# Kernel optimization log

Hardware: AMD Instinct MI355X
Metric: run time of the kernel (lower is better)

## Reference

```python
import jax, jax.numpy as jnp
import numpy as np

NH, D, MULT, NLAYER = 8, 512, 32, 3
N_INT = D * MULT // NH  # 2048 sparse-code dim per head
EPS = 1e-5
THETA = 2.0 ** 16
NUM_CLASSES = 2


def _ln(x):
    # LayerNorm over last dim, no affine (elementwise_affine=False), biased var
    m = jnp.mean(x, axis=-1, keepdims=True)
    v = jnp.mean((x - m) ** 2, axis=-1, keepdims=True)
    return (x - m) * jax.lax.rsqrt(v + EPS)


def _rotate_half(x):
    x1, x2 = jnp.split(x, 2, axis=-1)
    return jnp.concatenate((-x2, x1), axis=-1)


def _attn(Qs, V):
    # Qs: [B,nh,T,N] ReLU-sparse codes (Q == K), V: [B,1,T,D] raw hidden
    T = Qs.shape[2]
    half = 1.0 / (THETA ** (jnp.arange(0, N_INT, 2, dtype=jnp.float32) / N_INT))
    freqs = jnp.concatenate((half, half))                      # [N]
    ph = jnp.arange(T, dtype=jnp.float32)[:, None] * freqs[None, :]  # [T,N]
    QR = Qs * jnp.cos(ph) + _rotate_half(Qs) * jnp.sin(ph)
    scores = jnp.einsum('bhtn,bhsn->bhts', QR, QR)             # no softmax, no scaling
    mask = jnp.tril(jnp.ones((T, T), dtype=scores.dtype), k=-1)  # strictly causal
    scores = scores * mask
    return jnp.einsum('bhts,bsd->bhtd', scores, V[:, 0])       # [B,nh,T,D]


def setup_inputs():
    key = jax.random.key(0)
    ks = jax.random.split(key, 8)
    B, T, NA, F = 2, 1024, 93, 4
    in_dim, out_dim = NA * F, NA * NUM_CLASSES
    s = 0.02
    return dict(
        x=jax.random.normal(ks[0], (B, T, NA, F), dtype=jnp.float32),
        Wi=jax.random.normal(ks[1], (in_dim, D), dtype=jnp.float32) * s,
        bi=jnp.zeros((D,), jnp.float32),
        enc=jax.random.uniform(ks[2], (NH, D, N_INT), jnp.float32, -s, s),
        enc_v=jax.random.uniform(ks[3], (NH, D, N_INT), jnp.float32, -s, s),
        dec=jax.random.uniform(ks[4], (NH * N_INT, D), jnp.float32, -s, s),
        Wo=jax.random.normal(ks[5], (D, out_dim), dtype=jnp.float32) * s,
        bo=jnp.zeros((out_dim,), jnp.float32),
    )


def reference(x, Wi, bi, enc, enc_v, dec, Wo, bo):
    B, T, NA, F = x.shape
    h = _ln((x.reshape(B, T, NA * F) @ Wi + bi)[:, None])      # [B,1,T,D]
    for _ in range(NLAYER):
        h_res = h
        h_sp = jax.nn.relu(jnp.einsum('bxtd,hdn->bhtn', h, enc))      # [B,nh,T,N]
        yKV = _ln(_attn(h_sp, h))                                     # [B,nh,T,D]
        y_sp = jax.nn.relu(jnp.einsum('bhtd,hdn->bhtn', yKV, enc_v))  # [B,nh,T,N]
        xy = h_sp * y_sp                                              # gating
        # transpose(1,2).reshape(B,1,T,nh*N): head-major flatten of codes
        xy_flat = xy.transpose(0, 2, 1, 3).reshape(B, 1, T, NH * N_INT)
        h = _ln(h_res + _ln(xy_flat @ dec))                           # [B,1,T,D]
    out = h[:, 0] @ Wo + bo                                           # [B,T,NA*C]
    return out.reshape(B, T, NA, NUM_CLASSES)
```

## Files before the change

### kernel.cpp

```cpp
#include <hip/hip_runtime.h>

typedef __bf16 bf16;
typedef __attribute__((ext_vector_type(8))) __bf16 bf16x8;
typedef __attribute__((ext_vector_type(4))) float f32x4;

#define T_SEQ 1024
#define D_MODEL 512
#define N_INT 2048
#define NHEADS 8
#define IN_DIM 372
#define IN_PAD 384
#define OUT_DIM 186
#define OUT_PAD 256

__device__ inline void gld16(const bf16* g, bf16* l) {
  __builtin_amdgcn_global_load_lds((const __attribute__((address_space(1))) void*)g,
                                   (__attribute__((address_space(3))) void*)l, 16, 0, 0);
}

__device__ inline void block_sum2(float& a, float& b, float* red) {
#pragma unroll
  for (int o = 32; o > 0; o >>= 1) {
    a += __shfl_down(a, o, 64);
    b += __shfl_down(b, o, 64);
  }
  __syncthreads();
  if ((threadIdx.x & 63) == 0) {
    int w = threadIdx.x >> 6;
    red[2 * w] = a;
    red[2 * w + 1] = b;
  }
  __syncthreads();
  a = red[0] + red[2] + red[4] + red[6];
  b = red[1] + red[3] + red[5] + red[7];
}

__global__ __launch_bounds__(256) void transpose_cvt(const float* __restrict__ in,
                                                     bf16* __restrict__ out,
                                                     int rows, int cols) {
  __shared__ float tile[32][33];
  size_t zoff = (size_t)blockIdx.z * rows * cols;
  in += zoff;
  out += zoff;
  int c0 = blockIdx.x * 32, r0 = blockIdx.y * 32;
#pragma unroll
  for (int i = threadIdx.y; i < 32; i += 8)
    tile[i][threadIdx.x] = in[(size_t)(r0 + i) * cols + c0 + threadIdx.x];
  __syncthreads();
#pragma unroll
  for (int i = threadIdx.y; i < 32; i += 8)
    out[(size_t)(c0 + i) * rows + r0 + threadIdx.x] = (bf16)tile[threadIdx.x][i];
}

__global__ __launch_bounds__(256) void pad_trans(const float* __restrict__ in,
                                                 bf16* __restrict__ out,
                                                 int R, int C, int outLd) {
  __shared__ float tile[32][33];
  int c0 = blockIdx.x * 32, r0 = blockIdx.y * 32;
#pragma unroll
  for (int i = threadIdx.y; i < 32; i += 8) {
    int r = r0 + i, c = c0 + threadIdx.x;
    tile[i][threadIdx.x] = (r < R && c < C) ? in[(size_t)r * C + c] : 0.f;
  }
  __syncthreads();
#pragma unroll
  for (int i = threadIdx.y; i < 32; i += 8)
    out[(size_t)(c0 + i) * outLd + r0 + threadIdx.x] = (bf16)tile[threadIdx.x][i];
}

__global__ __launch_bounds__(256) void cvt_pad_x(const float* __restrict__ x,
                                                 bf16* __restrict__ xbf) {
  size_t r = blockIdx.x;
  for (int c = threadIdx.x; c < IN_PAD; c += 256)
    xbf[r * IN_PAD + c] = (c < IN_DIM) ? (bf16)x[r * IN_DIM + c] : (bf16)0.f;
}

__global__ __launch_bounds__(256) void rope_tables(float* __restrict__ ct, float* __restrict__ st) {
  int t = blockIdx.x;
  for (int i = threadIdx.x; i < 1024; i += 256) {
    float ph = (float)t * exp2f(-16.0f * (float)i * (1.0f / 1024.0f));
    ct[(size_t)t * 1024 + i] = cosf(ph);
    st[(size_t)t * 1024 + i] = sinf(ph);
  }
}

__global__ __launch_bounds__(256) void psum16(const bf16* __restrict__ part,
                                              float* __restrict__ zb) {
  size_t r = blockIdx.x;
  for (int cc = threadIdx.x; cc < 512; cc += 256) {
    float s = 0.f;
#pragma unroll
    for (int k = 0; k < 16; ++k)
      s += (float)part[((size_t)k << 19) + r * 512 + cc];
    zb[r * 512 + cc] = s;
  }
}

__global__ __launch_bounds__(256) void ln0(const float* __restrict__ zin,
                                           float* __restrict__ h, bf16* __restrict__ hbf,
                                           bf16* __restrict__ hT) {
  __shared__ float red[8];
  size_t r = blockIdx.x;
  int tid = threadIdx.x;
  float v0 = zin[r * 512 + tid], v1 = zin[r * 512 + tid + 256];
  float s = v0 + v1, s2 = v0 * v0 + v1 * v1;
  block_sum2(s, s2, red);
  float mean = s * (1.f / 512.f);
  float var = s2 * (1.f / 512.f) - mean * mean;
  float rs = rsqrtf(var + 1e-5f);
  float o0 = (v0 - mean) * rs, o1 = (v1 - mean) * rs;
  h[r * 512 + tid] = o0;
  h[r * 512 + tid + 256] = o1;
  hbf[r * 512 + tid] = (bf16)o0;
  hbf[r * 512 + tid + 256] = (bf16)o1;
  int b = (int)(r >> 10), t = (int)(r & (T_SEQ - 1));
  hT[((size_t)b * 512 + tid) * T_SEQ + t] = (bf16)o0;
  hT[((size_t)b * 512 + tid + 256) * T_SEQ + t] = (bf16)o1;
}

__global__ __launch_bounds__(256) void ln_rows(bf16* __restrict__ io) {
  const int wid = threadIdx.x >> 6, lane = threadIdx.x & 63;
  size_t r = (size_t)blockIdx.x * 4 + wid;
  bf16* p = io + r * 512 + lane * 8;
  bf16x8 v = *(const bf16x8*)p;
  float f[8], s = 0.f, s2 = 0.f;
#pragma unroll
  for (int j = 0; j < 8; ++j) {
    f[j] = (float)v[j];
    s += f[j];
    s2 += f[j] * f[j];
  }
#pragma unroll
  for (int o = 32; o > 0; o >>= 1) {
    s += __shfl_xor(s, o, 64);
    s2 += __shfl_xor(s2, o, 64);
  }
  float mean = s * (1.f / 512.f);
  float var = s2 * (1.f / 512.f) - mean * mean;
  float rs = rsqrtf(var + 1e-5f);
  bf16x8 o;
#pragma unroll
  for (int j = 0; j < 8; ++j) o[j] = (bf16)((f[j] - mean) * rs);
  *(bf16x8*)p = o;
}

__global__ __launch_bounds__(256) void ln_double(const float* __restrict__ zin,
                                                 float* __restrict__ h, bf16* __restrict__ hbf,
                                                 bf16* __restrict__ hT) {
  __shared__ float red[8];
  size_t r = blockIdx.x;
  int tid = threadIdx.x;
  float z0 = zin[r * 512 + tid], z1 = zin[r * 512 + tid + 256];
  float s = z0 + z1, s2 = z0 * z0 + z1 * z1;
  block_sum2(s, s2, red);
  float m1 = s * (1.f / 512.f);
  float v1_ = s2 * (1.f / 512.f) - m1 * m1;
  float rs1 = rsqrtf(v1_ + 1e-5f);
  float a0 = (z0 - m1) * rs1 + h[r * 512 + tid];
  float a1 = (z1 - m1) * rs1 + h[r * 512 + tid + 256];
  s = a0 + a1;
  s2 = a0 * a0 + a1 * a1;
  block_sum2(s, s2, red);
  float m2 = s * (1.f / 512.f);
  float v2_ = s2 * (1.f / 512.f) - m2 * m2;
  float rs2 = rsqrtf(v2_ + 1e-5f);
  float o0 = (a0 - m2) * rs2, o1 = (a1 - m2) * rs2;
  h[r * 512 + tid] = o0;
  h[r * 512 + tid + 256] = o1;
  hbf[r * 512 + tid] = (bf16)o0;
  hbf[r * 512 + tid + 256] = (bf16)o1;
  int b = (int)(r >> 10), t = (int)(r & (T_SEQ - 1));
  hT[((size_t)b * 512 + tid) * T_SEQ + t] = (bf16)o0;
  hT[((size_t)b * 512 + tid + 256) * T_SEQ + t] = (bf16)o1;
}

__global__ __launch_bounds__(256, 2) void g_hspr(const bf16* __restrict__ hbf_b,
                                                 const bf16* __restrict__ encT,
                                                 const float* __restrict__ ct,
                                                 const float* __restrict__ st,
                                                 bf16* __restrict__ hsp,
                                                 bf16* __restrict__ qr) {
  const int id = blockIdx.x;
  const int bz = id & 7;
  const int r_ = id >> 3;
  const int bi = r_ & 7;
  const int bj = r_ >> 3;

  const bf16* B0 = encT + (size_t)bz * N_INT * 512 + (size_t)(bj * 64) * 512;
  const bf16* B1 = B0 + (size_t)1024 * 512;

  const int tid = threadIdx.x;
  const int trow = tid >> 3, tq = tid & 7;
  const int sq = tq ^ (trow & 7);
  const bf16* ags = hbf_b + (size_t)(bi * 128 + trow) * 512 + sq * 8;
  const bf16* bgs0 = B0 + (size_t)trow * 512 + sq * 8;
  const bf16* bgs1 = B1 + (size_t)trow * 512 + sq * 8;

  __shared__ __align__(16) bf16 As[2][128 * 64];
  __shared__ __align__(16) bf16 Bs[2][2 * 64 * 64];
  const int so = tid * 8;

  const int lane = tid & 63, wid = tid >> 6;
  const int wr = wid >> 1, wc = wid & 1;
  const int fr = lane & 15, fg = lane >> 4;
  const int axor = fr & 7;

  f32x4 acc[4][2][2] = {};

  auto stage = [&](int buf, int kk) {
#pragma unroll
    for (int p = 0; p < 4; ++p)
      gld16(ags + (size_t)(p * 32) * 512 + kk, &As[buf][p * 2048 + so]);
    gld16(bgs0 + kk, &Bs[buf][0 * 2048 + so]);
    gld16(bgs0 + (size_t)32 * 512 + kk, &Bs[buf][1 * 2048 + so]);
    gld16(bgs1 + kk, &Bs[buf][2 * 2048 + so]);
    gld16(bgs1 + (size_t)32 * 512 + kk, &Bs[buf][3 * 2048 + so]);
  };

  stage(0, 0);
  asm volatile("s_waitcnt vmcnt(0)" ::: "memory");
  __builtin_amdgcn_s_barrier();

  for (int t = 0; t < 8; ++t) {
    const int cur = t & 1;
    if (t + 1 < 8) stage(cur ^ 1, (t + 1) << 6);

    __builtin_amdgcn_s_setprio(1);
#pragma unroll
    for (int s = 0; s < 2; ++s) {
      bf16x8 af[4], bfv[2][2];
#pragma unroll
      for (int m = 0; m < 4; ++m)
        af[m] = *(const bf16x8*)(&As[cur][(wr * 64 + m * 16 + fr) * 64 + (((s * 4 + fg) ^ axor) * 8)]);
#pragma unroll
      for (int pp = 0; pp < 2; ++pp)
#pragma unroll
        for (int n = 0; n < 2; ++n)
          bfv[pp][n] = *(const bf16x8*)(&Bs[cur][pp * 4096 + (wc * 32 + n * 16 + fr) * 64 + (((s * 4 + fg) ^ axor) * 8)]);
#pragma unroll
      for (int m = 0; m < 4; ++m)
#pragma unroll
        for (int n = 0; n < 2; ++n)
#pragma unroll
          for (int pp = 0; pp < 2; ++pp)
            acc[m][n][pp] = __builtin_amdgcn_mfma_f32_16x16x32_bf16(af[m], bfv[pp][n], acc[m][n][pp], 0, 0, 0);
    }
    __builtin_amdgcn_s_setprio(0);

    asm volatile("s_waitcnt vmcnt(0)" ::: "memory");
    __builtin_amdgcn_sched_barrier(0);
    __builtin_amdgcn_s_barrier();
    __builtin_amdgcn_sched_barrier(0);
  }

  const size_t hb = (size_t)bz * T_SEQ;
#pragma unroll
  for (int m = 0; m < 4; ++m) {
#pragma unroll
    for (int n = 0; n < 2; ++n) {
      int c = bj * 64 + wc * 32 + n * 16 + fr;
#pragma unroll
      for (int j = 0; j < 4; ++j) {
        int r = bi * 128 + wr * 64 + m * 16 + fg * 4 + j;
        float v0 = fmaxf(acc[m][n][0][j], 0.f);
        float v1 = fmaxf(acc[m][n][1][j], 0.f);
        float co = ct[(size_t)r * 1024 + c];
        float si = st[(size_t)r * 1024 + c];
        size_t base = (hb + r) * N_INT + c;
        hsp[base] = (bf16)v0;
        hsp[base + 1024] = (bf16)v1;
        qr[base] = (bf16)(v0 * co - v1 * si);
        qr[base + 1024] = (bf16)(v1 * co + v0 * si);
      }
    }
  }
}

template <int MODE, int GX, int TILE>
__device__ __forceinline__ void gemm_body(const bf16* __restrict__ Abase,
                                          const bf16* __restrict__ Bbase,
                                          const bf16* __restrict__ aux,
                                          const float* __restrict__ fbias,
                                          float* __restrict__ fout,
                                          bf16* __restrict__ bout) {
  const int id = blockIdx.x;
  int bz = 0, r_, chunk = 0;
  if constexpr (MODE >= 5) {
    r_ = id;
  } else if constexpr (MODE == 4) {
    r_ = id & 31;
    chunk = id >> 5;
  } else {
    bz = id & 7;
    r_ = id >> 3;
  }
  int bi, bj;
  if constexpr (MODE == 1) {
    int l = r_;
    float f = sqrtf(8.0f * (float)l + 1.0f);
    bi = (int)((f - 1.0f) * 0.5f);
    while ((bi + 1) * (bi + 2) / 2 <= l) ++bi;
    while (bi * (bi + 1) / 2 > l) --bi;
    bj = l - bi * (bi + 1) / 2;
  } else {
    bi = r_ % GX;
    bj = r_ / GX;
  }

  const bf16* A;
  const bf16* Bt;
  int lda, ldb, kend;
  if constexpr (MODE == 1) {
    A = Abase + (size_t)bz * T_SEQ * N_INT; lda = N_INT;
    Bt = A; ldb = N_INT;
    kend = N_INT;
  } else if constexpr (MODE == 2) {
    A = Abase + (size_t)bz * T_SEQ * T_SEQ; lda = T_SEQ;
    Bt = Bbase; ldb = T_SEQ;
    kend = (bi + 1) * TILE;
  } else if constexpr (MODE == 3) {
    A = Abase + (size_t)bz * T_SEQ * 512; lda = 512;
    Bt = Bbase + (size_t)bz * N_INT * 512; ldb = 512;
    kend = 512;
  } else if constexpr (MODE == 4) {
    A = Abase + (size_t)chunk * 1024; lda = 16384;
    Bt = Bbase + (size_t)chunk * 1024; ldb = 16384;
    kend = 1024;
  } else if constexpr (MODE == 5) {
    A = Abase; lda = IN_PAD;
    Bt = Bbase; ldb = IN_PAD;
    kend = IN_PAD;
  } else {
    A = Abase; lda = 512;
    Bt = Bbase; ldb = 512;
    kend = 512;
  }

  const int tid = threadIdx.x;
  constexpr int PASSES = TILE / 32;
  const int trow = tid >> 3, tq = tid & 7;
  const int sq = tq ^ (trow & 7);
  const bf16* ags = A + (size_t)(bi * TILE + trow) * lda + sq * 8;
  const bf16* bgs = Bt + (size_t)(bj * TILE + trow) * ldb + sq * 8;

  __shared__ __align__(16) bf16 As[2][TILE * 64];
  __shared__ __align__(16) bf16 Bs[2][TILE * 64];
  const int so = tid * 8;

  const int lane = tid & 63, wid = tid >> 6;
  const int wr = wid >> 1, wc = wid & 1;
  const int fr = lane & 15, fg = lane >> 4;
  const int axor = fr & 7;
  constexpr int MR = TILE / 32;

  f32x4 acc[MR][MR] = {};

  auto stage = [&](int buf, int kk) {
#pragma unroll
    for (int p = 0; p < PASSES; ++p) {
      gld16(ags + (size_t)(p * 32) * lda + kk, &As[buf][p * 2048 + so]);
      gld16(bgs + (size_t)(p * 32) * ldb + kk, &Bs[buf][p * 2048 + so]);
    }
  };

  const int nt = kend >> 6;
  stage(0, 0);
  asm volatile("s_waitcnt vmcnt(0)" ::: "memory");
  __builtin_amdgcn_s_barrier();

  for (int t = 0; t < nt; ++t) {
    const int cur = t & 1;
    if (t + 1 < nt) stage(cur ^ 1, (t + 1) << 6);

    __builtin_amdgcn_s_setprio(1);
#pragma unroll
    for (int s = 0; s < 2; ++s) {
      bf16x8 af[MR], bfv[MR];
#pragma unroll
      for (int m = 0; m < MR; ++m)
        af[m] = *(const bf16x8*)(&As[cur][(wr * (TILE / 2) + m * 16 + fr) * 64 + (((s * 4 + fg) ^ axor) * 8)]);
#pragma unroll
      for (int n = 0; n < MR; ++n)
        bfv[n] = *(const bf16x8*)(&Bs[cur][(wc * (TILE / 2) + n * 16 + fr) * 64 + (((s * 4 + fg) ^ axor) * 8)]);
#pragma unroll
      for (int m = 0; m < MR; ++m)
#pragma unroll
        for (int n = 0; n < MR; ++n)
          acc[m][n] = __builtin_amdgcn_mfma_f32_16x16x32_bf16(af[m], bfv[n], acc[m][n], 0, 0, 0);
    }
    __builtin_amdgcn_s_setprio(0);

    asm volatile("s_waitcnt vmcnt(0)" ::: "memory");
    __builtin_amdgcn_sched_barrier(0);
    __builtin_amdgcn_s_barrier();
    __builtin_amdgcn_sched_barrier(0);
  }

#pragma unroll
  for (int m = 0; m < MR; ++m) {
#pragma unroll
    for (int n = 0; n < MR; ++n) {
#pragma unroll
      for (int j = 0; j < 4; ++j) {
        int r = bi * TILE + wr * (TILE / 2) + m * 16 + fg * 4 + j;
        int c = bj * TILE + wc * (TILE / 2) + n * 16 + fr;
        float v = acc[m][n][j];
        if constexpr (MODE == 1) {
          bout[(size_t)bz * T_SEQ * T_SEQ + (size_t)r * T_SEQ + c] = (bf16)(c < r ? v : 0.f);
        } else if constexpr (MODE == 2) {
          bout[((size_t)bz * T_SEQ + r) * 512 + c] = (bf16)v;
        } else if constexpr (MODE == 3) {
          v = fmaxf(v, 0.f);
          float g = (float)aux[((size_t)bz * T_SEQ + r) * N_INT + c];
          bout[(size_t)r * 16384 + (size_t)bz * N_INT + c] = (bf16)(v * g);
        } else if constexpr (MODE == 4) {
          bout[((size_t)chunk << 19) + (size_t)r * 512 + c] = (bf16)v;
        } else if constexpr (MODE == 5) {
          fout[(size_t)r * 512 + c] = v + fbias[c];
        } else {
          if (c < OUT_DIM) fout[(size_t)r * OUT_DIM + c] = v + fbias[c];
        }
      }
    }
  }
}

__global__ __launch_bounds__(256, 4) void g_scores(const bf16* A, bf16* o) {
  gemm_body<1, 0, 64>(A, nullptr, nullptr, nullptr, nullptr, o);
}
__global__ __launch_bounds__(256, 4) void g_pv(const bf16* A, const bf16* B, bf16* o) {
  gemm_body<2, 16, 64>(A, B, nullptr, nullptr, nullptr, o);
}
__global__ __launch_bounds__(256, 2) void g_gate(const bf16* A, const bf16* B, const bf16* aux, bf16* o) {
  gemm_body<3, 8, 128>(A, B, aux, nullptr, nullptr, o);
}
__global__ __launch_bounds__(256, 2) void g_dec(const bf16* A, const bf16* B, bf16* o) {
  gemm_body<4, 8, 128>(A, B, nullptr, nullptr, nullptr, o);
}
__global__ __launch_bounds__(256, 2) void g_in(const bf16* A, const bf16* B, const float* bias, float* o) {
  gemm_body<5, 16, 128>(A, B, nullptr, bias, o, nullptr);
}
__global__ __launch_bounds__(256, 2) void g_out(const bf16* A, const bf16* B, const float* bias, float* o) {
  gemm_body<6, 16, 128>(A, B, nullptr, bias, o, nullptr);
}

extern "C" void kernel_launch(void* const* d_in, const int* in_sizes, int n_in,
                              void* d_out, int out_size, void* d_ws, size_t ws_size,
                              hipStream_t stream) {
  const float* x = (const float*)d_in[0];
  const float* Wi = (const float*)d_in[1];
  const float* bi = (const float*)d_in[2];
  const float* enc = (const float*)d_in[3];
  const float* encv = (const float*)d_in[4];
  const float* dec = (const float*)d_in[5];
  const float* Wo = (const float*)d_in[6];
  const float* bo = (const float*)d_in[7];
  float* out = (float*)d_out;

  const size_t NEED = 163840000;
  if (ws_size < NEED) return;

  char* w = (char*)d_ws;
  auto alloc = [&](size_t bytes) {
    char* p = w;
    w += (bytes + 255) & ~(size_t)255;
    return p;
  };
  bf16* encT = (bf16*)alloc((size_t)NHEADS * N_INT * 512 * 2);
  bf16* encvT = (bf16*)alloc((size_t)NHEADS * N_INT * 512 * 2);
  bf16* decT = (bf16*)alloc((size_t)512 * 16384 * 2);
  float* cost = (float*)alloc((size_t)T_SEQ * 1024 * 4);
  float* sint = (float*)alloc((size_t)T_SEQ * 1024 * 4);
  float* h = (float*)alloc((size_t)2048 * 512 * 4);
  bf16* hbf = (bf16*)alloc((size_t)2048 * 512 * 2);
  bf16* hT = (bf16*)alloc((size_t)2048 * 512 * 2);
  bf16* hsp = (bf16*)alloc((size_t)NHEADS * T_SEQ * N_INT * 2);
  bf16* qr = (bf16*)alloc((size_t)NHEADS * T_SEQ * N_INT * 2);
  bf16* S = (bf16*)alloc((size_t)NHEADS * T_SEQ * T_SEQ * 2);
  bf16* ykv = (bf16*)alloc((size_t)NHEADS * T_SEQ * 512 * 2);
  float* zbuf = (float*)alloc((size_t)2048 * 512 * 4);
  bf16* WoT = (bf16*)alloc((size_t)OUT_PAD * 512 * 2);
  bf16* xbf = S;
  bf16* WiT = S + 1048576;

  transpose_cvt<<<dim3(64, 16, 8), dim3(32, 8), 0, stream>>>(enc, encT, 512, N_INT);
  transpose_cvt<<<dim3(64, 16, 8), dim3(32, 8), 0, stream>>>(encv, encvT, 512, N_INT);
  transpose_cvt<<<dim3(16, 512, 1), dim3(32, 8), 0, stream>>>(dec, decT, 16384, 512);
  pad_trans<<<dim3(16, 12), dim3(32, 8), 0, stream>>>(Wi, WiT, IN_DIM, 512, IN_PAD);
  pad_trans<<<dim3(8, 16), dim3(32, 8), 0, stream>>>(Wo, WoT, 512, OUT_DIM, 512);
  cvt_pad_x<<<2048, 256, 0, stream>>>(x, xbf);
  rope_tables<<<1024, 256, 0, stream>>>(cost, sint);
  g_in<<<64, 256, 0, stream>>>(xbf, WiT, bi, zbuf);
  ln0<<<2048, 256, 0, stream>>>(zbuf, h, hbf, hT);

  for (int L = 0; L < 3; ++L) {
    for (int b = 0; b < 2; ++b) {
      const bf16* hbf_b = hbf + (size_t)b * T_SEQ * 512;
      const bf16* hT_b = hT + (size_t)b * 512 * T_SEQ;
      float* zbuf_b = zbuf + (size_t)b * T_SEQ * 512;
      g_hspr<<<1024, 256, 0, stream>>>(hbf_b, encT, cost, sint, hsp, qr);
      g_scores<<<1088, 256, 0, stream>>>(qr, S);
      g_pv<<<1024, 256, 0, stream>>>(S, hT_b, ykv);
      ln_rows<<<2048, 256, 0, stream>>>(ykv);
      g_gate<<<1024, 256, 0, stream>>>(ykv, encvT, hsp, qr);
      g_dec<<<512, 256, 0, stream>>>(qr, decT, S);
      psum16<<<1024, 256, 0, stream>>>(S, zbuf_b);
    }
    ln_double<<<2048, 256, 0, stream>>>(zbuf, h, hbf, hT);
  }
  g_out<<<32, 256, 0, stream>>>(hbf, WoT, bo, out);
}
```

Measured before the change: 1.029 ms.

## Enlarge GEMM tiles to 256-row 512-thread blocks and fuse partial-sum into double LN

All GEMM kernels and g_hspr move from 256-thread blocks with 64/128 tiles to 512-thread, 8-wave blocks with 256-row A tiles and 64/128-wide B tiles. Block-index mappings and grid sizes are rewritten to match, including the triangular score tiling. This raises operand reuse per LDS load and cuts redundant global traffic. The separate psum16 reduction and the per-layer ln_double are merged into one per-batch psum_lnd kernel, removing the fp32 zbuf round trip and one launch per layer. In exchange, LDS use per block is much higher and there are far fewer blocks (e.g. 160 for scores), which risks poorer occupancy and load balance across CUs.

```diff
diff --git a/kernel.cpp b/kernel.cpp
--- a/kernel.cpp
+++ b/kernel.cpp
@@ -81,18 +81,6 @@
     float ph = (float)t * exp2f(-16.0f * (float)i * (1.0f / 1024.0f));
     ct[(size_t)t * 1024 + i] = cosf(ph);
     st[(size_t)t * 1024 + i] = sinf(ph);
-  }
-}
-
-__global__ __launch_bounds__(256) void psum16(const bf16* __restrict__ part,
-                                              float* __restrict__ zb) {
-  size_t r = blockIdx.x;
-  for (int cc = threadIdx.x; cc < 512; cc += 256) {
-    float s = 0.f;
-#pragma unroll
-    for (int k = 0; k < 16; ++k)
-      s += (float)part[((size_t)k << 19) + r * 512 + cc];
-    zb[r * 512 + cc] = s;
   }
 }
 
@@ -144,20 +132,26 @@
   *(bf16x8*)p = o;
 }
 
-__global__ __launch_bounds__(256) void ln_double(const float* __restrict__ zin,
-                                                 float* __restrict__ h, bf16* __restrict__ hbf,
-                                                 bf16* __restrict__ hT) {
+__global__ __launch_bounds__(256) void psum_lnd(const bf16* __restrict__ part,
+                                                float* __restrict__ h, bf16* __restrict__ hbf,
+                                                bf16* __restrict__ hT, int b) {
   __shared__ float red[8];
-  size_t r = blockIdx.x;
+  int r = blockIdx.x;
   int tid = threadIdx.x;
-  float z0 = zin[r * 512 + tid], z1 = zin[r * 512 + tid + 256];
+  float z0 = 0.f, z1 = 0.f;
+#pragma unroll
+  for (int k = 0; k < 16; ++k) {
+    z0 += (float)part[((size_t)k << 19) + (size_t)r * 512 + tid];
+    z1 += (float)part[((size_t)k << 19) + (size_t)r * 512 + tid + 256];
+  }
   float s = z0 + z1, s2 = z0 * z0 + z1 * z1;
   block_sum2(s, s2, red);
   float m1 = s * (1.f / 512.f);
   float v1_ = s2 * (1.f / 512.f) - m1 * m1;
   float rs1 = rsqrtf(v1_ + 1e-5f);
-  float a0 = (z0 - m1) * rs1 + h[r * 512 + tid];
-  float a1 = (z1 - m1) * rs1 + h[r * 512 + tid + 256];
+  size_t R = (size_t)b * T_SEQ + r;
+  float a0 = (z0 - m1) * rs1 + h[R * 512 + tid];
+  float a1 = (z1 - m1) * rs1 + h[R * 512 + tid + 256];
   s = a0 + a1;
   s2 = a0 * a0 + a1 * a1;
   block_sum2(s, s2, red);
@@ -165,118 +159,15 @@
   float v2_ = s2 * (1.f / 512.f) - m2 * m2;
   float rs2 = rsqrtf(v2_ + 1e-5f);
   float o0 = (a0 - m2) * rs2, o1 = (a1 - m2) * rs2;
-  h[r * 512 + tid] = o0;
-  h[r * 512 + tid + 256] = o1;
-  hbf[r * 512 + tid] = (bf16)o0;
-  hbf[r * 512 + tid + 256] = (bf16)o1;
-  int b = (int)(r >> 10), t = (int)(r & (T_SEQ - 1));
-  hT[((size_t)b * 512 + tid) * T_SEQ + t] = (bf16)o0;
-  hT[((size_t)b * 512 + tid + 256) * T_SEQ + t] = (bf16)o1;
-}
-
-__global__ __launch_bounds__(256, 2) void g_hspr(const bf16* __restrict__ hbf_b,
-                                                 const bf16* __restrict__ encT,
-                                                 const float* __restrict__ ct,
-                                                 const float* __restrict__ st,
-                                                 bf16* __restrict__ hsp,
-                                                 bf16* __restrict__ qr) {
-  const int id = blockIdx.x;
-  const int bz = id & 7;
-  const int r_ = id >> 3;
-  const int bi = r_ & 7;
-  const int bj = r_ >> 3;
-
-  const bf16* B0 = encT + (size_t)bz * N_INT * 512 + (size_t)(bj * 64) * 512;
-  const bf16* B1 = B0 + (size_t)1024 * 512;
-
-  const int tid = threadIdx.x;
-  const int trow = tid >> 3, tq = tid & 7;
-  const int sq = tq ^ (trow & 7);
-  const bf16* ags = hbf_b + (size_t)(bi * 128 + trow) * 512 + sq * 8;
-  const bf16* bgs0 = B0 + (size_t)trow * 512 + sq * 8;
-  const bf16* bgs1 = B1 + (size_t)trow * 512 + sq * 8;
-
-  __shared__ __align__(16) bf16 As[2][128 * 64];
-  __shared__ __align__(16) bf16 Bs[2][2 * 64 * 64];
-  const int so = tid * 8;
-
-  const int lane = tid & 63, wid = tid >> 6;
-  const int wr = wid >> 1, wc = wid & 1;
-  const int fr = lane & 15, fg = lane >> 4;
-  const int axor = fr & 7;
-
-  f32x4 acc[4][2][2] = {};
-
-  auto stage = [&](int buf, int kk) {
-#pragma unroll
-    for (int p = 0; p < 4; ++p)
-      gld16(ags + (size_t)(p * 32) * 512 + kk, &As[buf][p * 2048 + so]);
-    gld16(bgs0 + kk, &Bs[buf][0 * 2048 + so]);
-    gld16(bgs0 + (size_t)32 * 512 + kk, &Bs[buf][1 * 2048 + so]);
-    gld16(bgs1 + kk, &Bs[buf][2 * 2048 + so]);
-    gld16(bgs1 + (size_t)32 * 512 + kk, &Bs[buf][3 * 2048 + so]);
-  };
-
-  stage(0, 0);
-  asm volatile("s_waitcnt vmcnt(0)" ::: "memory");
-  __builtin_amdgcn_s_barrier();
-
-  for (int t = 0; t < 8; ++t) {
-    const int cur = t & 1;
-    if (t + 1 < 8) stage(cur ^ 1, (t + 1) << 6);
-
-    __builtin_amdgcn_s_setprio(1);
-#pragma unroll
-    for (int s = 0; s < 2; ++s) {
-      bf16x8 af[4], bfv[2][2];
-#pragma unroll
-      for (int m = 0; m < 4; ++m)
-        af[m] = *(const bf16x8*)(&As[cur][(wr * 64 + m * 16 + fr) * 64 + (((s * 4 + fg) ^ axor) * 8)]);
-#pragma unroll
-      for (int pp = 0; pp < 2; ++pp)
-#pragma unroll
-        for (int n = 0; n < 2; ++n)
-          bfv[pp][n] = *(const bf16x8*)(&Bs[cur][pp * 4096 + (wc * 32 + n * 16 + fr) * 64 + (((s * 4 + fg) ^ axor) * 8)]);
-#pragma unroll
-      for (int m = 0; m < 4; ++m)
-#pragma unroll
-        for (int n = 0; n < 2; ++n)
-#pragma unroll
-          for (int pp = 0; pp < 2; ++pp)
-            acc[m][n][pp] = __builtin_amdgcn_mfma_f32_16x16x32_bf16(af[m], bfv[pp][n], acc[m][n][pp], 0, 0, 0);
-    }
-    __builtin_amdgcn_s_setprio(0);
-
-    asm volatile("s_waitcnt vmcnt(0)" ::: "memory");
-    __builtin_amdgcn_sched_barrier(0);
-    __builtin_amdgcn_s_barrier();
-    __builtin_amdgcn_sched_barrier(0);
-  }
-
-  const size_t hb = (size_t)bz * T_SEQ;
-#pragma unroll
-  for (int m = 0; m < 4; ++m) {
-#pragma unroll
-    for (int n = 0; n < 2; ++n) {
-      int c = bj * 64 + wc * 32 + n * 16 + fr;
-#pragma unroll
-      for (int j = 0; j < 4; ++j) {
-        int r = bi * 128 + wr * 64 + m * 16 + fg * 4 + j;
-        float v0 = fmaxf(acc[m][n][0][j], 0.f);
-        float v1 = fmaxf(acc[m][n][1][j], 0.f);
-        float co = ct[(size_t)r * 1024 + c];
-        float si = st[(size_t)r * 1024 + c];
-        size_t base = (hb + r) * N_INT + c;
-        hsp[base] = (bf16)v0;
-        hsp[base + 1024] = (bf16)v1;
-        qr[base] = (bf16)(v0 * co - v1 * si);
-        qr[base + 1024] = (bf16)(v1 * co + v0 * si);
-      }
-    }
-  }
-}
-
-template <int MODE, int GX, int TILE>
+  h[R * 512 + tid] = o0;
+  h[R * 512 + tid + 256] = o1;
+  hbf[R * 512 + tid] = (bf16)o0;
+  hbf[R * 512 + tid + 256] = (bf16)o1;
+  hT[((size_t)b * 512 + tid) * T_SEQ + r] = (bf16)o0;
+  hT[((size_t)b * 512 + tid + 256) * T_SEQ + r] = (bf16)o1;
+}
+
+template <int MODE, int TN>
 __device__ __forceinline__ void gemm_body(const bf16* __restrict__ Abase,
                                           const bf16* __restrict__ Bbase,
                                           const bf16* __restrict__ aux,
@@ -288,8 +179,8 @@
   if constexpr (MODE >= 5) {
     r_ = id;
   } else if constexpr (MODE == 4) {
-    r_ = id & 31;
-    chunk = id >> 5;
+    r_ = id & 15;
+    chunk = id >> 4;
   } else {
     bz = id & 7;
     r_ = id >> 3;
@@ -297,14 +188,18 @@
   int bi, bj;
   if constexpr (MODE == 1) {
     int l = r_;
-    float f = sqrtf(8.0f * (float)l + 1.0f);
-    bi = (int)((f - 1.0f) * 0.5f);
-    while ((bi + 1) * (bi + 2) / 2 <= l) ++bi;
-    while (bi * (bi + 1) / 2 > l) --bi;
-    bj = l - bi * (bi + 1) / 2;
+    bi = (int)sqrtf((float)l);
+    while ((bi + 1) * (bi + 2) <= l) ++bi;
+    while (bi * (bi + 1) > l) --bi;
+    bj = l - bi * (bi + 1);
+  } else if constexpr (MODE == 2) {
+    bi = r_ & 3; bj = r_ >> 2;
+  } else if constexpr (MODE == 3) {
+    bi = r_ & 3; bj = r_ >> 2;
+  } else if constexpr (MODE == 4) {
+    bi = r_ & 3; bj = r_ >> 2;
   } else {
-    bi = r_ % GX;
-    bj = r_ / GX;
+    bi = r_ & 7; bj = r_ >> 3;
   }
 
   const bf16* A;
@@ -317,7 +212,7 @@
   } else if constexpr (MODE == 2) {
     A = Abase + (size_t)bz * T_SEQ * T_SEQ; lda = T_SEQ;
     Bt = Bbase; ldb = T_SEQ;
-    kend = (bi + 1) * TILE;
+    kend = (bi + 1) * 256;
   } else if constexpr (MODE == 3) {
     A = Abase + (size_t)bz * T_SEQ * 512; lda = 512;
     Bt = Bbase + (size_t)bz * N_INT * 512; ldb = 512;
@@ -337,30 +232,30 @@
   }
 
   const int tid = threadIdx.x;
-  constexpr int PASSES = TILE / 32;
   const int trow = tid >> 3, tq = tid & 7;
   const int sq = tq ^ (trow & 7);
-  const bf16* ags = A + (size_t)(bi * TILE + trow) * lda + sq * 8;
-  const bf16* bgs = Bt + (size_t)(bj * TILE + trow) * ldb + sq * 8;
-
-  __shared__ __align__(16) bf16 As[2][TILE * 64];
-  __shared__ __align__(16) bf16 Bs[2][TILE * 64];
+  const bf16* ags = A + (size_t)(bi * 256 + trow) * lda + sq * 8;
+  const bf16* bgs = Bt + (size_t)(bj * TN + trow) * ldb + sq * 8;
+
+  __shared__ __align__(16) bf16 As[2][256 * 64];
+  __shared__ __align__(16) bf16 Bs[2][TN * 64];
   const int so = tid * 8;
 
   const int lane = tid & 63, wid = tid >> 6;
   const int wr = wid >> 1, wc = wid & 1;
   const int fr = lane & 15, fg = lane >> 4;
   const int axor = fr & 7;
-  constexpr int MR = TILE / 32;
-
-  f32x4 acc[MR][MR] = {};
+  constexpr int NR = TN / 32;
+
+  f32x4 acc[4][NR] = {};
 
   auto stage = [&](int buf, int kk) {
 #pragma unroll
-    for (int p = 0; p < PASSES; ++p) {
-      gld16(ags + (size_t)(p * 32) * lda + kk, &As[buf][p * 2048 + so]);
-      gld16(bgs + (size_t)(p * 32) * ldb + kk, &Bs[buf][p * 2048 + so]);
-    }
+    for (int p = 0; p < 4; ++p)
+      gld16(ags + (size_t)(p * 64) * lda + kk, &As[buf][p * 4096 + so]);
+#pragma unroll
+    for (int p = 0; p < TN / 64; ++p)
+      gld16(bgs + (size_t)(p * 64) * ldb + kk, &Bs[buf][p * 4096 + so]);
   };
 
   const int nt = kend >> 6;
@@ -375,17 +270,17 @@
     __builtin_amdgcn_s_setprio(1);
 #pragma unroll
     for (int s = 0; s < 2; ++s) {
-      bf16x8 af[MR], bfv[MR];
-#pragma unroll
-      for (int m = 0; m < MR; ++m)
-        af[m] = *(const bf16x8*)(&As[cur][(wr * (TILE / 2) + m * 16 + fr) * 64 + (((s * 4 + fg) ^ axor) * 8)]);
-#pragma unroll
-      for (int n = 0; n < MR; ++n)
-        bfv[n] = *(const bf16x8*)(&Bs[cur][(wc * (TILE / 2) + n * 16 + fr) * 64 + (((s * 4 + fg) ^ axor) * 8)]);
-#pragma unroll
-      for (int m = 0; m < MR; ++m)
-#pragma unroll
-        for (int n = 0; n < MR; ++n)
+      bf16x8 af[4], bfv[NR];
+#pragma unroll
+      for (int m = 0; m < 4; ++m)
+        af[m] = *(const bf16x8*)(&As[cur][(wr * 64 + m * 16 + fr) * 64 + (((s * 4 + fg) ^ axor) * 8)]);
+#pragma unroll
+      for (int n = 0; n < NR; ++n)
+        bfv[n] = *(const bf16x8*)(&Bs[cur][(wc * (TN / 2) + n * 16 + fr) * 64 + (((s * 4 + fg) ^ axor) * 8)]);
+#pragma unroll
+      for (int m = 0; m < 4; ++m)
+#pragma unroll
+        for (int n = 0; n < NR; ++n)
           acc[m][n] = __builtin_amdgcn_mfma_f32_16x16x32_bf16(af[m], bfv[n], acc[m][n], 0, 0, 0);
     }
     __builtin_amdgcn_s_setprio(0);
@@ -397,13 +292,13 @@
   }
 
 #pragma unroll
-  for (int m = 0; m < MR; ++m) {
-#pragma unroll
-    for (int n = 0; n < MR; ++n) {
+  for (int m = 0; m < 4; ++m) {
+#pragma unroll
+    for (int n = 0; n < NR; ++n) {
+      int c = bj * TN + wc * (TN / 2) + n * 16 + fr;
 #pragma unroll
       for (int j = 0; j < 4; ++j) {
-        int r = bi * TILE + wr * (TILE / 2) + m * 16 + fg * 4 + j;
-        int c = bj * TILE + wc * (TILE / 2) + n * 16 + fr;
+        int r = bi * 256 + wr * 64 + m * 16 + fg * 4 + j;
         float v = acc[m][n][j];
         if constexpr (MODE == 1) {
           bout[(size_t)bz * T_SEQ * T_SEQ + (size_t)r * T_SEQ + c] = (bf16)(c < r ? v : 0.f);
@@ -425,23 +320,126 @@
   }
 }
 
-__global__ __launch_bounds__(256, 4) void g_scores(const bf16* A, bf16* o) {
-  gemm_body<1, 0, 64>(A, nullptr, nullptr, nullptr, nullptr, o);
-}
-__global__ __launch_bounds__(256, 4) void g_pv(const bf16* A, const bf16* B, bf16* o) {
-  gemm_body<2, 16, 64>(A, B, nullptr, nullptr, nullptr, o);
-}
-__global__ __launch_bounds__(256, 2) void g_gate(const bf16* A, const bf16* B, const bf16* aux, bf16* o) {
-  gemm_body<3, 8, 128>(A, B, aux, nullptr, nullptr, o);
-}
-__global__ __launch_bounds__(256, 2) void g_dec(const bf16* A, const bf16* B, bf16* o) {
-  gemm_body<4, 8, 128>(A, B, nullptr, nullptr, nullptr, o);
-}
-__global__ __launch_bounds__(256, 2) void g_in(const bf16* A, const bf16* B, const float* bias, float* o) {
-  gemm_body<5, 16, 128>(A, B, nullptr, bias, o, nullptr);
-}
-__global__ __launch_bounds__(256, 2) void g_out(const bf16* A, const bf16* B, const float* bias, float* o) {
-  gemm_body<6, 16, 128>(A, B, nullptr, bias, o, nullptr);
+__global__ __launch_bounds__(512, 2) void g_scores(const bf16* A, bf16* o) {
+  gemm_body<1, 128>(A, nullptr, nullptr, nullptr, nullptr, o);
+}
+__global__ __launch_bounds__(512, 2) void g_pv(const bf16* A, const bf16* B, bf16* o) {
+  gemm_body<2, 64>(A, B, nullptr, nullptr, nullptr, o);
+}
+__global__ __launch_bounds__(512, 2) void g_gate(const bf16* A, const bf16* B, const bf16* aux, bf16* o) {
+  gemm_body<3, 128>(A, B, aux, nullptr, nullptr, o);
+}
+__global__ __launch_bounds__(512, 2) void g_dec(const bf16* A, const bf16* B, bf16* o) {
+  gemm_body<4, 128>(A, B, nullptr, nullptr, nullptr, o);
+}
+__global__ __launch_bounds__(512, 2) void g_in(const bf16* A, const bf16* B, const float* bias, float* o) {
+  gemm_body<5, 128>(A, B, nullptr, bias, o, nullptr);
+}
+__global__ __launch_bounds__(512, 2) void g_out(const bf16* A, const bf16* B, const float* bias, float* o) {
+  gemm_body<6, 128>(A, B, nullptr, bias, o, nullptr);
+}
+
+__global__ __launch_bounds__(512, 2) void g_hspr(const bf16* __restrict__ hbf_b,
+                                                 const bf16* __restrict__ encT,
+                                                 const float* __restrict__ ct,
+                                                 const float* __restrict__ st,
+                                                 bf16* __restrict__ hsp,
+                                                 bf16* __restrict__ qr) {
+  const int id = blockIdx.x;
+  const int bz = id & 7;
+  const int r_ = id >> 3;
+  const int bi = r_ & 3;
+  const int bjp = r_ >> 2;
+
+  const bf16* B0 = encT + (size_t)bz * N_INT * 512 + (size_t)(bjp * 128) * 512;
+  const bf16* B1 = B0 + (size_t)1024 * 512;
+
+  const int tid = threadIdx.x;
+  const int trow = tid >> 3, tq = tid & 7;
+  const int sq = tq ^ (trow & 7);
+  const bf16* ags = hbf_b + (size_t)(bi * 256 + trow) * 512 + sq * 8;
+  const bf16* bgs0 = B0 + (size_t)trow * 512 + sq * 8;
+  const bf16* bgs1 = B1 + (size_t)trow * 512 + sq * 8;
+
+  __shared__ __align__(16) bf16 As[2][256 * 64];
+  __shared__ __align__(16) bf16 Bs[2][2 * 128 * 64];
+  const int so = tid * 8;
+
+  const int lane = tid & 63, wid = tid >> 6;
+  const int wr = wid >> 1, wc = wid & 1;
+  const int fr = lane & 15, fg = lane >> 4;
+  const int axor = fr & 7;
+
+  f32x4 acc[4][4][2] = {};
+
+  auto stage = [&](int buf, int kk) {
+#pragma unroll
+    for (int p = 0; p < 4; ++p)
+      gld16(ags + (size_t)(p * 64) * 512 + kk, &As[buf][p * 4096 + so]);
+#pragma unroll
+    for (int p = 0; p < 2; ++p) {
+      gld16(bgs0 + (size_t)(p * 64) * 512 + kk, &Bs[buf][p * 4096 + so]);
+      gld16(bgs1 + (size_t)(p * 64) * 512 + kk, &Bs[buf][8192 + p * 4096 + so]);
+    }
+  };
+
+  stage(0, 0);
+  asm volatile("s_waitcnt vmcnt(0)" ::: "memory");
+  __builtin_amdgcn_s_barrier();
+
+  for (int t = 0; t < 8; ++t) {
+    const int cur = t & 1;
+    if (t + 1 < 8) stage(cur ^ 1, (t + 1) << 6);
+
+    __builtin_amdgcn_s_setprio(1);
+#pragma unroll
+    for (int s = 0; s < 2; ++s) {
+      bf16x8 af[4], bfv[4][2];
+#pragma unroll
+      for (int m = 0; m < 4; ++m)
+        af[m] = *(const bf16x8*)(&As[cur][(wr * 64 + m * 16 + fr) * 64 + (((s * 4 + fg) ^ axor) * 8)]);
+#pragma unroll
+      for (int pp = 0; pp < 2; ++pp)
+#pragma unroll
+        for (int n = 0; n < 4; ++n)
+          bfv[n][pp] = *(const bf16x8*)(&Bs[cur][pp * 8192 + (wc * 64 + n * 16 + fr) * 64 + (((s * 4 + fg) ^ axor) * 8)]);
+#pragma unroll
+      for (int m = 0; m < 4; ++m)
+#pragma unroll
+        for (int n = 0; n < 4; ++n)
+#pragma unroll
+          for (int pp = 0; pp < 2; ++pp)
+            acc[m][n][pp] = __builtin_amdgcn_mfma_f32_16x16x32_bf16(af[m], bfv[n][pp], acc[m][n][pp], 0, 0, 0);
+    }
+    __builtin_amdgcn_s_setprio(0);
+
+    asm volatile("s_waitcnt vmcnt(0)" ::: "memory");
+    __builtin_amdgcn_sched_barrier(0);
+    __builtin_amdgcn_s_barrier();
+    __builtin_amdgcn_sched_barrier(0);
+  }
+
+  const size_t hb = (size_t)bz * T_SEQ;
+#pragma unroll
+  for (int m = 0; m < 4; ++m) {
+#pragma unroll
+    for (int n = 0; n < 4; ++n) {
+      int c = bjp * 128 + wc * 64 + n * 16 + fr;
+#pragma unroll
+      for (int j = 0; j < 4; ++j) {
+        int r = bi * 256 + wr * 64 + m * 16 + fg * 4 + j;
+        float v0 = fmaxf(acc[m][n][0][j], 0.f);
+        float v1 = fmaxf(acc[m][n][1][j], 0.f);
+        float co = ct[(size_t)r * 1024 + c];
+        float si = st[(size_t)r * 1024 + c];
+        size_t base = (hb + r) * N_INT + c;
+        hsp[base] = (bf16)v0;
+        hsp[base + 1024] = (bf16)v1;
+        qr[base] = (bf16)(v0 * co - v1 * si);
+        qr[base + 1024] = (bf16)(v1 * co + v0 * si);
+      }
+    }
+  }
 }
 
 extern "C" void kernel_launch(void* const* d_in, const int* in_sizes, int n_in,
@@ -490,23 +488,21 @@
   pad_trans<<<dim3(8, 16), dim3(32, 8), 0, stream>>>(Wo, WoT, 512, OUT_DIM, 512);
   cvt_pad_x<<<2048, 256, 0, stream>>>(x, xbf);
   rope_tables<<<1024, 256, 0, stream>>>(cost, sint);
-  g_in<<<64, 256, 0, stream>>>(xbf, WiT, bi, zbuf);
+  g_in<<<32, 512, 0, stream>>>(xbf, WiT, bi, zbuf);
   ln0<<<2048, 256, 0, stream>>>(zbuf, h, hbf, hT);
 
   for (int L = 0; L < 3; ++L) {
     for (int b = 0; b < 2; ++b) {
       const bf16* hbf_b = hbf + (size_t)b * T_SEQ * 512;
       const bf16* hT_b = hT + (size_t)b * 512 * T_SEQ;
-      float* zbuf_b = zbuf + (size_t)b * T_SEQ * 512;
-      g_hspr<<<1024, 256, 0, stream>>>(hbf_b, encT, cost, sint, hsp, qr);
-      g_scores<<<1088, 256, 0, stream>>>(qr, S);
-      g_pv<<<1024, 256, 0, stream>>>(S, hT_b, ykv);
+      g_hspr<<<256, 512, 0, stream>>>(hbf_b, encT, cost, sint, hsp, qr);
+      g_scores<<<160, 512, 0, stream>>>(qr, S);
+      g_pv<<<256, 512, 0, stream>>>(S, hT_b, ykv);
       ln_rows<<<2048, 256, 0, stream>>>(ykv);
-      g_gate<<<1024, 256, 0, stream>>>(ykv, encvT, hsp, qr);
-      g_dec<<<512, 256, 0, stream>>>(qr, decT, S);
-      psum16<<<1024, 256, 0, stream>>>(S, zbuf_b);
+      g_gate<<<512, 512, 0, stream>>>(ykv, encvT, hsp, qr);
+      g_dec<<<256, 512, 0, stream>>>(qr, decT, S);
+      psum_lnd<<<1024, 256, 0, stream>>>(S, h, hbf, hT, b);
     }
-    ln_double<<<2048, 256, 0, stream>>>(zbuf, h, hbf, hT);
-  }
-  g_out<<<32, 256, 0, stream>>>(hbf, WoT, bo, out);
-}
+  }
+  g_out<<<16, 512, 0, stream>>>(hbf, WoT, bo, out);
+}
```

Result: slower. 1.149 ms (+11.6%).
